# Kernel optimization log

Hardware: AMD Instinct MI355X
Metric: run time of the kernel (lower is better)

## Reference

```python
import jax, jax.numpy as jnp
import numpy as np

HID = 10
IN_DIM = 256
B, H, W = 8, 96, 96


def _conv(x, w, b=None, pad=0):
    y = jax.lax.conv_general_dilated(x, w, (1, 1), [(pad, pad), (pad, pad)],
                                     dimension_numbers=('NCHW', 'OIHW', 'NCHW'))
    return y if b is None else y + b[None, :, None, None]


def _bn(x, g, b):
    # eval-mode InPlaceABN(Sync) with identity running stats -> per-channel affine
    return x * g[None, :, None, None] + b[None, :, None, None]


def _branch(x, w1, g1, b1, w2, g2, b2):
    # Conv3x3 -> BN -> ReLU -> Conv1x1 -> BN -> ReLU  (relation / comp_u / comp_l)
    y = jax.nn.relu(_bn(_conv(x, w1, pad=1), g1, b1))
    return jax.nn.relu(_bn(_conv(y, w2), g2, b2))


def _gru(x, h, gw, gb, cw, cg, cb):
    # ConvGRU with 1x1 kernels
    gates = _conv(jnp.concatenate([x, h], axis=1), gw, gb)
    r = jax.nn.sigmoid(gates[:, 0:1])
    u = jax.nn.sigmoid(gates[:, 1:2])
    cnm = jax.nn.relu(_bn(_conv(jnp.concatenate([x, r * h], axis=1), cw), cg, cb))
    return (1.0 - u) * h + u * cnm


def setup_inputs():
    key = jax.random.key(0)
    ks = iter(jax.random.split(key, 48))

    def nrm(shape, s=0.05):
        return jax.random.normal(next(ks), shape, jnp.float32) * s

    inp = {
        'f_nodes': jax.random.normal(next(ks), (2, B, HID, H, W), jnp.float32),
        'h_nodes': jax.random.normal(next(ks), (3, B, HID, H, W), jnp.float32),
        'p_nodes': jax.random.normal(next(ks), (7, B, HID, H, W), jnp.float32),
        'xh': jax.random.normal(next(ks), (B, IN_DIM, H, W), jnp.float32),
        'f_atts': jax.random.uniform(next(ks), (2, B, 1, H, W), jnp.float32),
        'p_atts': jax.random.uniform(next(ks), (7, B, 1, H, W), jnp.float32),
        # Decomposition.decomp_att: Conv3x3(257->256)+BN+ReLU, Conv1x1(256->2)+bias
        'da_w1': nrm((IN_DIM, IN_DIM + 1, 3, 3)),
        'da_g1': jnp.ones((IN_DIM,), jnp.float32),
        'da_b1': jnp.zeros((IN_DIM,), jnp.float32),
        'da_w2': nrm((2, IN_DIM, 1, 1)),
        'da_b2': jnp.zeros((2,), jnp.float32),
    }
    # relation (shared across children), comp_u, comp_l: Conv3x3(20->10)+BN+ReLU, Conv1x1(10->10)+BN+ReLU
    for p in ('rel', 'cu', 'cl'):
        inp[p + '_w1'] = nrm((HID, 2 * HID, 3, 3))
        inp[p + '_g1'] = jnp.ones((HID,), jnp.float32)
        inp[p + '_b1'] = jnp.zeros((HID,), jnp.float32)
        inp[p + '_w2'] = nrm((HID, HID, 1, 1))
        inp[p + '_g2'] = jnp.ones((HID,), jnp.float32)
        inp[p + '_b2'] = jnp.zeros((HID,), jnp.float32)
    # 3 ConvGRUs (cls_h), 1x1 kernels, stacked on leading dim
    inp['gru_gw'] = nrm((3, 2, 2 * HID, 1, 1))
    inp['gru_gb'] = jnp.zeros((3, 2), jnp.float32)
    inp['gru_cw'] = nrm((3, HID, 2 * HID, 1, 1))
    inp['gru_cg'] = jnp.ones((3, HID), jnp.float32)
    inp['gru_cb'] = jnp.zeros((3, HID), jnp.float32)
    return inp


def reference(f_nodes, h_nodes, p_nodes, xh, f_atts, p_atts,
              da_w1, da_g1, da_b1, da_w2, da_b2,
              rel_w1, rel_g1, rel_b1, rel_w2, rel_g2, rel_b2,
              cu_w1, cu_g1, cu_b1, cu_w2, cu_g2, cu_b2,
              cl_w1, cl_g1, cl_b1, cl_w2, cl_g2, cl_b2,
              gru_gw, gru_gb, gru_cw, gru_cg, gru_cb):
    parent, parent_att = f_nodes[1], f_atts[1]
    # Decomposition of full-body node into 2 half nodes
    dm = _conv(jnp.concatenate([parent_att, xh], axis=1), da_w1, pad=1)
    dm = jax.nn.relu(_bn(dm, da_g1, da_b1))
    dm = _conv(dm, da_w2, da_b2)  # [B, 2, H, W] decomposition map
    datt = jax.nn.softmax(dm, axis=1)
    decomp = [_branch(jnp.concatenate([parent * datt[:, i:i + 1] * parent_att,
                                       h_nodes[1 + i]], axis=1),
                      rel_w1, rel_g1, rel_b1, rel_w2, rel_g2, rel_b2)
              for i in range(2)]
    # node 0: background
    n0 = _gru(f_nodes[0] + p_nodes[0], h_nodes[0],
              gru_gw[0], gru_gb[0], gru_cw[0], gru_cg[0], gru_cb[0])
    # node 1: upper half = composition(upper parts 1-4) + decomposition
    up = jnp.sum(p_nodes[1:5], axis=0) * jnp.sum(p_atts[1:5], axis=0)
    comp_u = _branch(jnp.concatenate([h_nodes[1], up], axis=1),
                     cu_w1, cu_g1, cu_b1, cu_w2, cu_g2, cu_b2)
    n1 = _gru(comp_u + decomp[0], h_nodes[1],
              gru_gw[1], gru_gb[1], gru_cw[1], gru_cg[1], gru_cb[1])
    # node 2: lower half = composition(lower parts 5-6) + decomposition
    lo = jnp.sum(p_nodes[5:7], axis=0) * jnp.sum(p_atts[5:7], axis=0)
    comp_l = _branch(jnp.concatenate([h_nodes[2], lo], axis=1),
                     cl_w1, cl_g1, cl_b1, cl_w2, cl_g2, cl_b2)
    n2 = _gru(comp_l + decomp[1], h_nodes[2],
              gru_gw[2], gru_gb[2], gru_cw[2], gru_cg[2], gru_cb[2])
    return (jnp.stack([n0, n1, n2]), dm)
```

## Files before the change

kernel.cpp:

```cpp
#include <hip/hip_runtime.h>
#include <cstddef>
#include <cstdint>

constexpr int Bn    = 8;
constexpr int Hn    = 96;
constexpr int Wn    = 96;
constexpr int HWn   = Hn * Wn;
constexpr int BHWn  = Bn * HWn;
constexpr int B10HW = Bn * 10 * HWn;

constexpr int XP_COLS        = 100;
constexpr int XP_ROWS        = 100;
constexpr int XP_PLANE       = XP_ROWS * XP_COLS;
constexpr int XP_PLANE_BYTES = XP_PLANE * 16;
constexpr int XP_OCT         = 36;

using short8  = __attribute__((ext_vector_type(8))) short;
using ushort8 = __attribute__((ext_vector_type(8))) unsigned short;
using float4v = __attribute__((ext_vector_type(4))) float;

__device__ __forceinline__ unsigned short f2bf(float f) {
    unsigned u = __builtin_bit_cast(unsigned, f);
    u += 0x7FFFu + ((u >> 16) & 1u);
    return (unsigned short)(u >> 16);
}

__device__ __forceinline__ void async16(const void* g, void* l) {
    auto gp = (__attribute__((address_space(1))) unsigned int*)(uintptr_t)g;
    auto lp = (__attribute__((address_space(3))) unsigned int*)(unsigned)(uintptr_t)l;
    __builtin_amdgcn_global_load_lds(gp, lp, 16, 0, 0);
}

struct BranchW  { const float *w1, *g1, *b1, *w2, *g2, *b2; };
struct BranchW3 { BranchW p[3]; };

struct ConvSmem   { short xs[3][4][194][8]; float part[4][64][2]; };
struct BranchSmem {
    float xt[20][10][34];
    float paSum[340];
    float wlt[9 * 20 * 12];
    float w2l[100], g1l[10], b1l[10], g2l[10], b2l[10];
};
struct GruSmem    { float gwl[40], cwl[200], gbl[2], cgl[10], cbl[10]; };
union FusedSmem { ConvSmem c; BranchSmem b; GruSmem g; };

constexpr int PACKW_BLOCKS = 2592;

__global__ void k_pack(const float* __restrict__ w1, short* __restrict__ wpk,
                       const float* __restrict__ xh, const float* __restrict__ patt,
                       ushort* __restrict__ xp)
{
    if (blockIdx.x < PACKW_BLOCKS) {
        const int o = blockIdx.x * 256 + threadIdx.x;
        const int j    = o & 7;
        const int lane = (o >> 3) & 63;
        const int q    = (o >> 9) & 15;
        const int t    = o >> 13;
        const int co   = q * 16 + (lane & 15);
        const int ci   = (t / 9) * 32 + ((lane >> 4) & 3) * 8 + j;
        const int tap  = t % 9;
        const float f  = (ci < 257) ? w1[((size_t)co * 257 + ci) * 9 + tap] : 0.f;
        wpk[o] = (short)f2bf(f);
    } else {
        const int g  = (blockIdx.x - PACKW_BLOCKS) * 256 + threadIdx.x;
        const int cw = g % XP_COLS;
        int t = g / XP_COLS;
        const int rh = t % XP_ROWS; t /= XP_ROWS;
        const int o  = t % XP_OCT;
        const int b  = t / XP_OCT;
        const int hh = rh - 1, ww = cw - 1;
        const bool inb = ((unsigned)hh < (unsigned)Hn) & ((unsigned)ww < (unsigned)Wn);
        const int off = hh * Wn + ww;
        ushort8 v;
        #pragma unroll
        for (int j = 0; j < 8; ++j) {
            const int ci = o * 8 + j;
            float f = 0.f;
            if (inb && ci < 257)
                f = (ci == 0) ? patt[b * HWn + off]
                              : xh[((size_t)b * 256 + (ci - 1)) * HWn + off];
            v[j] = f2bf(f);
        }
        *(ushort8*)&xp[(size_t)g * 8] = v;
    }
}

__global__ void k_packw(const float* __restrict__ w1, short* __restrict__ wpk)
{
    const int o = blockIdx.x * 256 + threadIdx.x;
    if (o >= 663552) return;
    const int j    = o & 7;
    const int lane = (o >> 3) & 63;
    const int q    = (o >> 9) & 15;
    const int t    = o >> 13;
    const int co   = q * 16 + (lane & 15);
    const int ci   = (t / 9) * 32 + ((lane >> 4) & 3) * 8 + j;
    const int tap  = t % 9;
    const float f  = (ci < 257) ? w1[((size_t)co * 257 + ci) * 9 + tap] : 0.f;
    wpk[o] = (short)f2bf(f);
}

__device__ __forceinline__ void branch_body(
    BranchSmem& S, int z, int bx, int tid, const BranchW3& P,
    const float* __restrict__ parent, const float* __restrict__ h_nodes,
    const float* __restrict__ s01, const float* __restrict__ pn,
    const float* __restrict__ pa, float* __restrict__ bout)
{
    const int pi = (z < 2) ? 0 : (z - 1);
    const BranchW& Pw = P.p[pi];
    for (int idx = tid; idx < 2160; idx += 256) {
        const int co = idx % 12, rem = idx / 12, ci = rem % 20, tap = rem / 20;
        S.wlt[idx] = (co < 10) ? Pw.w1[(co * 20 + ci) * 9 + tap] : 0.f;
    }
    if (tid < 100) S.w2l[tid] = Pw.w2[tid];
    if (tid < 10) {
        S.g1l[tid] = Pw.g1[tid]; S.b1l[tid] = Pw.b1[tid];
        S.g2l[tid] = Pw.g2[tid]; S.b2l[tid] = Pw.b2[tid];
    }

    const int tw = bx % 3, th = (bx / 3) % 12, b = bx / 36;
    const int h0 = th * 8, w0 = tw * 32;

    const float* Ab;
    const float* sc = nullptr;
    const float* Bb = nullptr;
    int k0 = 0, k1 = -1;
    if (z == 0)      { Ab = parent; sc = s01;        Bb = h_nodes + (size_t)1 * B10HW; }
    else if (z == 1) { Ab = parent; sc = s01 + BHWn; Bb = h_nodes + (size_t)2 * B10HW; }
    else if (z == 2) { Ab = h_nodes + (size_t)1 * B10HW; k0 = 1; k1 = 4; }
    else             { Ab = h_nodes + (size_t)2 * B10HW; k0 = 5; k1 = 6; }

    if (z >= 2) {
        for (int idx = tid; idx < 340; idx += 256) {
            const int col = idx % 34, row = idx / 34;
            const int hh = h0 - 1 + row, ww = w0 - 1 + col;
            float s = 0.f;
            if (((unsigned)hh < (unsigned)Hn) & ((unsigned)ww < (unsigned)Wn)) {
                const int off = hh * Wn + ww;
                for (int k = k0; k <= k1; ++k)
                    s += pa[(size_t)(k * Bn + b) * HWn + off];
            }
            S.paSum[idx] = s;
        }
    }
    __syncthreads();

    for (int idx = tid; idx < 6800; idx += 256) {
        const int col = idx % 34, rem = idx / 34, row = rem % 10, ch = rem / 10;
        const int hh = h0 - 1 + row, ww = w0 - 1 + col;
        float v = 0.f;
        if (((unsigned)hh < (unsigned)Hn) & ((unsigned)ww < (unsigned)Wn)) {
            const int off = hh * Wn + ww;
            if (ch < 10) {
                v = Ab[((size_t)b * 10 + ch) * HWn + off];
                if (sc) v *= sc[b * HWn + off];
            } else if (z < 2) {
                v = Bb[((size_t)b * 10 + (ch - 10)) * HWn + off];
            } else {
                float s = 0.f;
                for (int k = k0; k <= k1; ++k)
                    s += pn[((size_t)(k * Bn + b) * 10 + (ch - 10)) * HWn + off];
                v = s * S.paSum[row * 34 + col];
            }
        }
        ((float*)S.xt)[idx] = v;
    }
    __syncthreads();

    const int r = tid >> 5, c = tid & 31;
    float a0 = 0, a1 = 0, a2 = 0, a3 = 0, a4 = 0, a5 = 0, a6 = 0, a7 = 0, a8 = 0, a9 = 0;
    #pragma unroll
    for (int tap = 0; tap < 9; ++tap) {
        const int kh = tap / 3, kw = tap % 3;
        #pragma unroll
        for (int ci = 0; ci < 20; ++ci) {
            const float xv = S.xt[ci][r + kh][c + kw];
            const float4 wA = *(const float4*)&S.wlt[(tap * 20 + ci) * 12];
            const float4 wB = *(const float4*)&S.wlt[(tap * 20 + ci) * 12 + 4];
            const float2 wC = *(const float2*)&S.wlt[(tap * 20 + ci) * 12 + 8];
            a0 = fmaf(wA.x, xv, a0); a1 = fmaf(wA.y, xv, a1);
            a2 = fmaf(wA.z, xv, a2); a3 = fmaf(wA.w, xv, a3);
            a4 = fmaf(wB.x, xv, a4); a5 = fmaf(wB.y, xv, a5);
            a6 = fmaf(wB.z, xv, a6); a7 = fmaf(wB.w, xv, a7);
            a8 = fmaf(wC.x, xv, a8); a9 = fmaf(wC.y, xv, a9);
        }
    }
    float acc[10] = {a0, a1, a2, a3, a4, a5, a6, a7, a8, a9};
    float y[10];
    #pragma unroll
    for (int co = 0; co < 10; ++co)
        y[co] = fmaxf(fmaf(acc[co], S.g1l[co], S.b1l[co]), 0.f);
    const int hw = (h0 + r) * Wn + (w0 + c);
    #pragma unroll
    for (int co = 0; co < 10; ++co) {
        float s = 0.f;
        #pragma unroll
        for (int i = 0; i < 10; ++i) s = fmaf(S.w2l[co * 10 + i], y[i], s);
        s = fmaxf(fmaf(s, S.g2l[co], S.b2l[co]), 0.f);
        bout[(size_t)z * B10HW + ((size_t)b * 10 + co) * HWn + hw] = s;
    }
}

__device__ __forceinline__ void gru_body(
    GruSmem& S, int z, int bx, int tid,
    const float* __restrict__ f_nodes, const float* __restrict__ h_nodes,
    const float* __restrict__ p_nodes, const float* __restrict__ bout,
    const float* __restrict__ gw, const float* __restrict__ gb,
    const float* __restrict__ cw, const float* __restrict__ cg,
    const float* __restrict__ cb, float* __restrict__ out)
{
    if (tid < 40)  S.gwl[tid] = gw[z * 40 + tid];
    if (tid < 200) S.cwl[tid] = cw[z * 200 + tid];
    if (tid < 2)   S.gbl[tid] = gb[z * 2 + tid];
    if (tid < 10) {
        S.cgl[tid] = cg[z * 10 + tid];
        S.cbl[tid] = cb[z * 10 + tid];
    }
    __syncthreads();

    const int p = bx * 256 + tid;
    const int b = p / HWn, hw = p % HWn;
    float x[10], h[10];
    #pragma unroll
    for (int c = 0; c < 10; ++c) {
        const size_t idx = ((size_t)b * 10 + c) * HWn + hw;
        if (z == 0)      x[c] = f_nodes[idx] + p_nodes[idx];
        else if (z == 1) x[c] = bout[(size_t)2 * B10HW + idx] + bout[idx];
        else             x[c] = bout[(size_t)3 * B10HW + idx] + bout[(size_t)1 * B10HW + idx];
        h[c] = h_nodes[(size_t)z * B10HW + idx];
    }
    float g0 = S.gbl[0], g1 = S.gbl[1];
    #pragma unroll
    for (int c = 0; c < 10; ++c) {
        g0 = fmaf(S.gwl[c],      x[c], g0);
        g0 = fmaf(S.gwl[10 + c], h[c], g0);
        g1 = fmaf(S.gwl[20 + c], x[c], g1);
        g1 = fmaf(S.gwl[30 + c], h[c], g1);
    }
    const float r = 1.f / (1.f + expf(-g0));
    const float u = 1.f / (1.f + expf(-g1));
    #pragma unroll
    for (int o = 0; o < 10; ++o) {
        float s = 0.f;
        #pragma unroll
        for (int c = 0; c < 10; ++c) {
            s = fmaf(S.cwl[o * 20 + c],      x[c],     s);
            s = fmaf(S.cwl[o * 20 + 10 + c], r * h[c], s);
        }
        s = fmaxf(fmaf(s, S.cgl[o], S.cbl[o]), 0.f);
        out[(size_t)z * B10HW + ((size_t)b * 10 + o) * HWn + hw] =
            (1.f - u) * h[o] + u * s;
    }
}

constexpr int CONV_BLOCKS = 1152;

__global__ __launch_bounds__(256, 3)
void k_fused(const char* __restrict__ xp, const float* __restrict__ patt,
             const short* __restrict__ wpk, const float* __restrict__ g1,
             const float* __restrict__ b1, const float* __restrict__ w2,
             const float* __restrict__ db2,
             float* __restrict__ dm_out, float* __restrict__ s01,
             BranchW3 P, const float* __restrict__ parent,
             const float* __restrict__ h_nodes, const float* __restrict__ pn,
             const float* __restrict__ pa, float* __restrict__ bout,
             const float* __restrict__ f_nodes, const float* __restrict__ p_nodes,
             const float* __restrict__ gw, const float* __restrict__ gb,
             const float* __restrict__ cw, const float* __restrict__ cg,
             const float* __restrict__ cb, float* __restrict__ out)
{
    __shared__ __align__(16) FusedSmem sm;
    const int tid = threadIdx.x;
    const int bxg = blockIdx.x;

    if (bxg >= CONV_BLOCKS) {
        const int r = bxg - CONV_BLOCKS;
        if (r < 576) {
            const int z = (r < 288) ? 2 : 3;
            branch_body(sm.b, z, (r < 288) ? r : r - 288, tid, P, parent,
                        h_nodes, s01, pn, pa, bout);
        } else {
            gru_body(sm.g, 0, r - 576, tid, f_nodes, h_nodes, p_nodes, bout,
                     gw, gb, cw, cg, cb, out);
        }
        return;
    }

    const int lane = tid & 63;
    const int wid  = tid >> 6;
    const int bx   = bxg;
    const int b    = bx & 7;
    const int r2   = bx >> 3;
    const int wseg = r2 % 3;
    const int hb   = r2 / 3;
    const int h0   = hb * 2, w0 = wseg * 32;
    const int am   = lane & 15;
    const int aq   = lane >> 4;

    int poff[3];
    #pragma unroll
    for (int it = 0; it < 3; ++it) {
        const int pos = it * 64 + lane;
        const int row = pos / 34, col = pos - row * 34;
        poff[it] = ((h0 + row) * XP_COLS + (w0 + col)) * 16;
    }
    const char* xpb = xp + ((size_t)b * XP_OCT + wid) * XP_PLANE_BYTES;

    float4v acc[4][4];
    #pragma unroll
    for (int i = 0; i < 4; ++i)
        #pragma unroll
        for (int j = 0; j < 4; ++j)
            acc[i][j] = float4v{0.f, 0.f, 0.f, 0.f};

    int arow[4], acol[4];
    #pragma unroll
    for (int mt = 0; mt < 4; ++mt) {
        const int m = mt * 16 + am;
        arow[mt] = m >> 5;
        acol[mt] = m & 31;
    }

    auto stageX = [&](int cb, int buf) {
        const char* src = xpb + (size_t)cb * (4 * XP_PLANE_BYTES);
        #pragma unroll
        for (int it = 0; it < 3; ++it)
            async16(src + poff[it], &sm.c.xs[buf][wid][it * 64][0]);
    };

    const short8* wp = (const short8*)wpk;
    const int qb = wid * 4;

    auto loadB = [&](int t, short8 (&dst)[4]) {
        #pragma unroll
        for (int nt = 0; nt < 4; ++nt)
            dst[nt] = wp[((size_t)t * 16 + qb + nt) * 64 + lane];
    };

    stageX(0, 0);
    stageX(1, 1);
    short8 bfr[3][4];
    loadB(0, bfr[0]);
    loadB(1, bfr[1]);

    for (int cb = 0; cb < 9; ++cb) {
        __builtin_amdgcn_sched_barrier(0);
        if (cb < 8) asm volatile("s_waitcnt vmcnt(3)" ::: "memory");
        else        asm volatile("s_waitcnt vmcnt(0)" ::: "memory");
        __builtin_amdgcn_s_barrier();
        __builtin_amdgcn_sched_barrier(0);
        if (cb < 7) stageX(cb + 2, (cb + 2) % 3);

        const int buf = cb % 3;
        #pragma unroll
        for (int tap = 0; tap < 9; ++tap) {
            const int t  = cb * 9 + tap;
            const int tl = (t + 2 <= 80) ? (t + 2) : 80;
            loadB(tl, bfr[(tap + 2) % 3]);
            const int kh = tap / 3, kw = tap % 3;
            short8 afr[4];
            #pragma unroll
            for (int mt = 0; mt < 4; ++mt) {
                const int pos = (arow[mt] + kh) * 34 + (acol[mt] + kw);
                afr[mt] = *(const short8*)&sm.c.xs[buf][aq][pos][0];
            }
            __builtin_amdgcn_s_setprio(1);
            #pragma unroll
            for (int mt = 0; mt < 4; ++mt)
                #pragma unroll
                for (int nt = 0; nt < 4; ++nt)
                    acc[mt][nt] = __builtin_amdgcn_mfma_f32_16x16x32_bf16(
                        afr[mt], bfr[tap % 3][nt], acc[mt][nt], 0, 0, 0);
            __builtin_amdgcn_s_setprio(0);
        }
    }

    float gv[4], bv[4], wa[4], wbv[4];
    #pragma unroll
    for (int nt = 0; nt < 4; ++nt) {
        const int co = wid * 64 + nt * 16 + am;
        gv[nt]  = g1[co];
        bv[nt]  = b1[co];
        wa[nt]  = w2[co];
        wbv[nt] = w2[256 + co];
    }
    #pragma unroll
    for (int mt = 0; mt < 4; ++mt) {
        #pragma unroll
        for (int reg = 0; reg < 4; ++reg) {
            float s0 = 0.f, s1 = 0.f;
            #pragma unroll
            for (int nt = 0; nt < 4; ++nt) {
                const float y = fmaxf(fmaf(acc[mt][nt][reg], gv[nt], bv[nt]), 0.f);
                s0 = fmaf(wa[nt], y, s0);
                s1 = fmaf(wbv[nt], y, s1);
            }
            #pragma unroll
            for (int off = 1; off < 16; off <<= 1) {
                s0 += __shfl_xor(s0, off, 64);
                s1 += __shfl_xor(s1, off, 64);
            }
            if (am == 0) {
                const int m = mt * 16 + aq * 4 + reg;
                sm.c.part[wid][m][0] = s0;
                sm.c.part[wid][m][1] = s1;
            }
        }
    }
    __syncthreads();
    if (tid < 64) {
        const int m = tid, r = m >> 5, c = m & 31;
        const int off = (h0 + r) * Wn + (w0 + c);
        float d0 = sm.c.part[0][m][0] + sm.c.part[1][m][0] + sm.c.part[2][m][0]
                 + sm.c.part[3][m][0] + db2[0];
        float d1 = sm.c.part[0][m][1] + sm.c.part[1][m][1] + sm.c.part[2][m][1]
                 + sm.c.part[3][m][1] + db2[1];
        dm_out[(size_t)(b * 2) * HWn + off]     = d0;
        dm_out[(size_t)(b * 2 + 1) * HWn + off] = d1;
        const float mx = fmaxf(d0, d1);
        const float e0 = expf(d0 - mx), e1 = expf(d1 - mx);
        const float pa2 = patt[b * HWn + off];
        const float inv = pa2 / (e0 + e1);
        s01[b * HWn + off]        = e0 * inv;
        s01[BHWn + b * HWn + off] = e1 * inv;
    }
}

__global__ __launch_bounds__(256)
void k_branch01(BranchW3 P, const float* __restrict__ parent,
                const float* __restrict__ h_nodes, const float* __restrict__ s01,
                const float* __restrict__ pn, const float* __restrict__ pa,
                float* __restrict__ bout)
{
    __shared__ __align__(16) BranchSmem S;
    branch_body(S, blockIdx.y, blockIdx.x, threadIdx.x, P, parent, h_nodes,
                s01, pn, pa, bout);
}

__global__ void k_gru12(const float* __restrict__ f_nodes, const float* __restrict__ h_nodes,
                        const float* __restrict__ p_nodes, const float* __restrict__ bout,
                        const float* __restrict__ gw, const float* __restrict__ gb,
                        const float* __restrict__ cw, const float* __restrict__ cg,
                        const float* __restrict__ cb, float* __restrict__ out)
{
    __shared__ GruSmem S;
    gru_body(S, blockIdx.y + 1, blockIdx.x, threadIdx.x, f_nodes, h_nodes,
             p_nodes, bout, gw, gb, cw, cg, cb, out);
}

__global__ __launch_bounds__(256)
void k_branch_all(BranchW3 P, const float* __restrict__ parent,
                  const float* __restrict__ h_nodes, const float* __restrict__ s01,
                  const float* __restrict__ pn, const float* __restrict__ pa,
                  float* __restrict__ bout)
{
    __shared__ __align__(16) BranchSmem S;
    branch_body(S, blockIdx.y, blockIdx.x, threadIdx.x, P, parent, h_nodes,
                s01, pn, pa, bout);
}

__global__ void k_gru_all(const float* __restrict__ f_nodes, const float* __restrict__ h_nodes,
                          const float* __restrict__ p_nodes, const float* __restrict__ bout,
                          const float* __restrict__ gw, const float* __restrict__ gb,
                          const float* __restrict__ cw, const float* __restrict__ cg,
                          const float* __restrict__ cb, float* __restrict__ out)
{
    __shared__ GruSmem S;
    gru_body(S, blockIdx.y, blockIdx.x, threadIdx.x, f_nodes, h_nodes,
             p_nodes, bout, gw, gb, cw, cg, cb, out);
}

__global__ __launch_bounds__(256, 3)
void k_bigconv3_f(const float* __restrict__ xh, const float* __restrict__ patt,
                  const short* __restrict__ wpk, const float* __restrict__ g1,
                  const float* __restrict__ b1, const float* __restrict__ w2,
                  const float* __restrict__ db2,
                  float* __restrict__ dm_out, float* __restrict__ s01)
{
    __shared__ __align__(16) short xs[2][4][137][8];
    __shared__ float part[4][64][2];

    const int tid  = threadIdx.x;
    const int lane = tid & 63;
    const int wid  = tid >> 6;
    const int bx   = blockIdx.x;
    const int b    = bx & 7;
    const int r2   = bx >> 3;
    const int wseg = r2 % 3;
    const int hb   = r2 / 3;
    const int h0   = hb * 2, w0 = wseg * 32;
    const int am   = lane & 15;
    const int aq   = lane >> 4;

    float4v acc[4][4];
    #pragma unroll
    for (int i = 0; i < 4; ++i)
        #pragma unroll
        for (int j = 0; j < 4; ++j)
            acc[i][j] = float4v{0.f, 0.f, 0.f, 0.f};

    int arow[4], acol[4];
    #pragma unroll
    for (int mt = 0; mt < 4; ++mt) {
        const int m = mt * 16 + am;
        arow[mt] = m >> 5;
        acol[mt] = m & 31;
    }

    auto stageX = [&](int cb, int buf) {
        const int cig0 = cb * 32 + wid * 8;
        for (int pos = lane; pos < 136; pos += 64) {
            const int row = pos / 34, col = pos % 34;
            const int hh = h0 - 1 + row, ww = w0 - 1 + col;
            const bool inb = ((unsigned)hh < (unsigned)Hn) & ((unsigned)ww < (unsigned)Wn);
            const int off = hh * Wn + ww;
            ushort8 v;
            #pragma unroll
            for (int j = 0; j < 8; ++j) {
                const int ci = cig0 + j;
                float f = 0.f;
                if (inb && ci < 257)
                    f = (ci == 0) ? patt[b * HWn + off]
                                  : xh[((size_t)b * 256 + (ci - 1)) * HWn + off];
                v[j] = f2bf(f);
            }
            *(ushort8*)&xs[buf][wid][pos][0] = v;
        }
    };

    const short8* wp = (const short8*)wpk;
    const int qb = wid * 4;

    stageX(0, 0);
    short8 bfr[4], bnx[4];
    #pragma unroll
    for (int nt = 0; nt < 4; ++nt)
        bfr[nt] = wp[(size_t)(qb + nt) * 64 + lane];
    __syncthreads();

    for (int cb = 0; cb < 9; ++cb) {
        const int buf = cb & 1;
        for (int tap = 0; tap < 9; ++tap) {
            const int t = cb * 9 + tap;
            if (t < 80) {
                #pragma unroll
                for (int nt = 0; nt < 4; ++nt)
                    bnx[nt] = wp[((size_t)(t + 1) * 16 + qb + nt) * 64 + lane];
            }
            const int kh = tap / 3, kw = tap % 3;
            short8 afr[4];
            #pragma unroll
            for (int mt = 0; mt < 4; ++mt) {
                const int pos = (arow[mt] + kh) * 34 + (acol[mt] + kw);
                afr[mt] = *(const short8*)&xs[buf][aq][pos][0];
            }
            #pragma unroll
            for (int mt = 0; mt < 4; ++mt)
                #pragma unroll
                for (int nt = 0; nt < 4; ++nt)
                    acc[mt][nt] = __builtin_amdgcn_mfma_f32_16x16x32_bf16(
                        afr[mt], bfr[nt], acc[mt][nt], 0, 0, 0);
            #pragma unroll
            for (int nt = 0; nt < 4; ++nt) bfr[nt] = bnx[nt];
        }
        if (cb < 8) stageX(cb + 1, buf ^ 1);
        __syncthreads();
    }

    float gv[4], bv[4], wa[4], wbv[4];
    #pragma unroll
    for (int nt = 0; nt < 4; ++nt) {
        const int co = wid * 64 + nt * 16 + am;
        gv[nt]  = g1[co];
        bv[nt]  = b1[co];
        wa[nt]  = w2[co];
        wbv[nt] = w2[256 + co];
    }
    #pragma unroll
    for (int mt = 0; mt < 4; ++mt) {
        #pragma unroll
        for (int reg = 0; reg < 4; ++reg) {
            float s0 = 0.f, s1 = 0.f;
            #pragma unroll
            for (int nt = 0; nt < 4; ++nt) {
                const float y = fmaxf(fmaf(acc[mt][nt][reg], gv[nt], bv[nt]), 0.f);
                s0 = fmaf(wa[nt], y, s0);
                s1 = fmaf(wbv[nt], y, s1);
            }
            #pragma unroll
            for (int off = 1; off < 16; off <<= 1) {
                s0 += __shfl_xor(s0, off, 64);
                s1 += __shfl_xor(s1, off, 64);
            }
            if (am == 0) {
                const int m = mt * 16 + aq * 4 + reg;
                part[wid][m][0] = s0;
                part[wid][m][1] = s1;
            }
        }
    }
    __syncthreads();
    if (tid < 64) {
        const int m = tid, r = m >> 5, c = m & 31;
        const int off = (h0 + r) * Wn + (w0 + c);
        float d0 = part[0][m][0] + part[1][m][0] + part[2][m][0] + part[3][m][0] + db2[0];
        float d1 = part[0][m][1] + part[1][m][1] + part[2][m][1] + part[3][m][1] + db2[1];
        dm_out[(size_t)(b * 2) * HWn + off]     = d0;
        dm_out[(size_t)(b * 2 + 1) * HWn + off] = d1;
        const float mx = fmaxf(d0, d1);
        const float e0 = expf(d0 - mx), e1 = expf(d1 - mx);
        const float pa = patt[b * HWn + off];
        const float inv = pa / (e0 + e1);
        s01[b * HWn + off]        = e0 * inv;
        s01[BHWn + b * HWn + off] = e1 * inv;
    }
}

extern "C" void kernel_launch(void* const* d_in, const int* in_sizes, int n_in,
                              void* d_out, int out_size, void* d_ws, size_t ws_size,
                              hipStream_t stream)
{
    (void)in_sizes; (void)n_in; (void)out_size;

    const float* f_nodes = (const float*)d_in[0];
    const float* h_nodes = (const float*)d_in[1];
    const float* p_nodes = (const float*)d_in[2];
    const float* xh      = (const float*)d_in[3];
    const float* f_atts  = (const float*)d_in[4];
    const float* p_atts  = (const float*)d_in[5];
    const float* da_w1   = (const float*)d_in[6];
    const float* da_g1   = (const float*)d_in[7];
    const float* da_b1   = (const float*)d_in[8];
    const float* da_w2   = (const float*)d_in[9];
    const float* da_b2   = (const float*)d_in[10];

    BranchW3 P;
    for (int i = 0; i < 3; ++i) {
        P.p[i].w1 = (const float*)d_in[11 + 6 * i + 0];
        P.p[i].g1 = (const float*)d_in[11 + 6 * i + 1];
        P.p[i].b1 = (const float*)d_in[11 + 6 * i + 2];
        P.p[i].w2 = (const float*)d_in[11 + 6 * i + 3];
        P.p[i].g2 = (const float*)d_in[11 + 6 * i + 4];
        P.p[i].b2 = (const float*)d_in[11 + 6 * i + 5];
    }
    const float* gru_gw = (const float*)d_in[29];
    const float* gru_gb = (const float*)d_in[30];
    const float* gru_cw = (const float*)d_in[31];
    const float* gru_cg = (const float*)d_in[32];
    const float* gru_cb = (const float*)d_in[33];

    float* out    = (float*)d_out;
    float* dm_out = out + (size_t)3 * B10HW;

    float* ws   = (float*)d_ws;
    float* s01  = ws;
    float* bout = s01 + 2 * BHWn;
    short* wpk  = (short*)bout;
    const size_t XP_OFF_B = ((size_t)(2 * BHWn) + 4 * (size_t)B10HW) * 4;
    char*  xp   = (char*)d_ws + XP_OFF_B;
    const size_t WS_NEED = XP_OFF_B + (size_t)Bn * XP_OCT * XP_PLANE_BYTES;
    const bool use_packed = ws_size >= WS_NEED;

    const float* patt   = f_atts + BHWn;
    const float* parent = f_nodes + B10HW;

    if (use_packed) {
        k_pack<<<dim3(PACKW_BLOCKS + 11250), 256, 0, stream>>>(da_w1, wpk, xh, patt,
                                                               (ushort*)xp);
        k_fused<<<dim3(CONV_BLOCKS + 576 + 288), 256, 0, stream>>>(
            xp, patt, wpk, da_g1, da_b1, da_w2, da_b2, dm_out, s01,
            P, parent, h_nodes, p_nodes, p_atts, bout,
            f_nodes, p_nodes, gru_gw, gru_gb, gru_cw, gru_cg, gru_cb, out);
        k_branch01<<<dim3(288, 2), 256, 0, stream>>>(P, parent, h_nodes, s01,
                                                     p_nodes, p_atts, bout);
        k_gru12<<<dim3(288, 2), 256, 0, stream>>>(f_nodes, h_nodes, p_nodes, bout,
                                                  gru_gw, gru_gb, gru_cw, gru_cg,
                                                  gru_cb, out);
    } else {
        k_packw<<<dim3(2592), 256, 0, stream>>>(da_w1, wpk);
        k_bigconv3_f<<<dim3(1152), 256, 0, stream>>>(xh, patt, wpk, da_g1, da_b1,
                                                     da_w2, da_b2, dm_out, s01);
        k_branch_all<<<dim3(288, 4), 256, 0, stream>>>(P, parent, h_nodes, s01,
                                                       p_nodes, p_atts, bout);
        k_gru_all<<<dim3(288, 3), 256, 0, stream>>>(f_nodes, h_nodes, p_nodes, bout,
                                                    gru_gw, gru_gb, gru_cw, gru_cg,
                                                    gru_cb, out);
    }
}
```

Baseline: 360.2 us.

## Split attention channel out of bf16 MFMA conv into separate fp32 rank-1 term

The 257-channel 3x3 conv had been padded to 288 input channels (9 chunks of 32), and the extra attention channel alone forced a ninth MFMA chunk. The attention channel now gets its own packed fp32 weights and is staged into LDS per block, then added to the accumulators as a 9-tap scalar FMA after the MFMA loop. The main loop therefore runs 8 chunks over exactly 256 channels, and the packed input shrinks from 36 to 32 octets, cutting pack traffic and MFMA work by about a ninth. The cost is extra scalar FMAs and LDS reads in the epilogue, plus more register pressure from the 36 per-thread weights.

After: 367.8 us. +2.1%, slower.

```diff
diff --git a/kernel.cpp b/kernel.cpp
--- a/kernel.cpp
+++ b/kernel.cpp
@@ -13,7 +13,7 @@
 constexpr int XP_ROWS        = 100;
 constexpr int XP_PLANE       = XP_ROWS * XP_COLS;
 constexpr int XP_PLANE_BYTES = XP_PLANE * 16;
-constexpr int XP_OCT         = 36;
+constexpr int XP_OCT         = 32;
 
 using short8  = __attribute__((ext_vector_type(8))) short;
 using ushort8 = __attribute__((ext_vector_type(8))) unsigned short;
@@ -34,7 +34,11 @@
 struct BranchW  { const float *w1, *g1, *b1, *w2, *g2, *b2; };
 struct BranchW3 { BranchW p[3]; };
 
-struct ConvSmem   { short xs[3][4][194][8]; float part[4][64][2]; };
+struct ConvSmem {
+    short xs[3][4][194][8];
+    float part[4][64][2];
+    float pt[4][34];
+};
 struct BranchSmem {
     float xt[20][10][34];
     float paSum[340];
@@ -44,11 +48,13 @@
 struct GruSmem    { float gwl[40], cwl[200], gbl[2], cgl[10], cbl[10]; };
 union FusedSmem { ConvSmem c; BranchSmem b; GruSmem g; };
 
-constexpr int PACKW_BLOCKS = 2592;
+constexpr int PACKW_BLOCKS  = 2304;
+constexpr int PACKPAT_BLOCKS = 9;
+constexpr int PACKX_BLOCKS  = 10000;
 
 __global__ void k_pack(const float* __restrict__ w1, short* __restrict__ wpk,
-                       const float* __restrict__ xh, const float* __restrict__ patt,
-                       ushort* __restrict__ xp)
+                       float* __restrict__ wpat,
+                       const float* __restrict__ xh, ushort* __restrict__ xp)
 {
     if (blockIdx.x < PACKW_BLOCKS) {
         const int o = blockIdx.x * 256 + threadIdx.x;
@@ -57,12 +63,18 @@
         const int q    = (o >> 9) & 15;
         const int t    = o >> 13;
         const int co   = q * 16 + (lane & 15);
-        const int ci   = (t / 9) * 32 + ((lane >> 4) & 3) * 8 + j;
+        const int ci   = (t / 9) * 32 + ((lane >> 4) & 3) * 8 + j + 1;
         const int tap  = t % 9;
-        const float f  = (ci < 257) ? w1[((size_t)co * 257 + ci) * 9 + tap] : 0.f;
-        wpk[o] = (short)f2bf(f);
+        wpk[o] = (short)f2bf(w1[((size_t)co * 257 + ci) * 9 + tap]);
+    } else if (blockIdx.x < PACKW_BLOCKS + PACKPAT_BLOCKS) {
+        const int idx = (blockIdx.x - PACKW_BLOCKS) * 256 + threadIdx.x;
+        if (idx < 2304) {
+            const int co = idx / 9, tap = idx % 9;
+            wpat[idx] = w1[(size_t)co * 257 * 9 + tap];
+        }
     } else {
-        const int g  = (blockIdx.x - PACKW_BLOCKS) * 256 + threadIdx.x;
+        const int g  = (blockIdx.x - PACKW_BLOCKS - PACKPAT_BLOCKS) * 256
+                     + threadIdx.x;
         const int cw = g % XP_COLS;
         int t = g / XP_COLS;
         const int rh = t % XP_ROWS; t /= XP_ROWS;
@@ -75,10 +87,7 @@
         #pragma unroll
         for (int j = 0; j < 8; ++j) {
             const int ci = o * 8 + j;
-            float f = 0.f;
-            if (inb && ci < 257)
-                f = (ci == 0) ? patt[b * HWn + off]
-                              : xh[((size_t)b * 256 + (ci - 1)) * HWn + off];
+            float f = inb ? xh[((size_t)b * 256 + ci) * HWn + off] : 0.f;
             v[j] = f2bf(f);
         }
         *(ushort8*)&xp[(size_t)g * 8] = v;
@@ -257,7 +266,8 @@
 
 __global__ __launch_bounds__(256, 3)
 void k_fused(const char* __restrict__ xp, const float* __restrict__ patt,
-             const short* __restrict__ wpk, const float* __restrict__ g1,
+             const short* __restrict__ wpk, const float* __restrict__ wpat,
+             const float* __restrict__ g1,
              const float* __restrict__ b1, const float* __restrict__ w2,
              const float* __restrict__ db2,
              float* __restrict__ dm_out, float* __restrict__ s01,
@@ -286,9 +296,9 @@
         return;
     }
 
+    const int bx   = bxg;
     const int lane = tid & 63;
     const int wid  = tid >> 6;
-    const int bx   = bxg;
     const int b    = bx & 7;
     const int r2   = bx >> 3;
     const int wseg = r2 % 3;
@@ -297,6 +307,16 @@
     const int am   = lane & 15;
     const int aq   = lane >> 4;
 
+    for (int idx = tid; idx < 136; idx += 256) {
+        const int row = idx / 34, col = idx % 34;
+        const int hh = h0 - 1 + row, ww = w0 - 1 + col;
+        float v = 0.f;
+        if (((unsigned)hh < (unsigned)Hn) & ((unsigned)ww < (unsigned)Wn))
+            v = patt[b * HWn + hh * Wn + ww];
+        sm.c.pt[row][col] = v;
+    }
+    asm volatile("s_waitcnt lgkmcnt(0)" ::: "memory");
+
     int poff[3];
     #pragma unroll
     for (int it = 0; it < 3; ++it) {
@@ -343,19 +363,19 @@
     loadB(0, bfr[0]);
     loadB(1, bfr[1]);
 
-    for (int cb = 0; cb < 9; ++cb) {
+    for (int cb = 0; cb < 8; ++cb) {
         __builtin_amdgcn_sched_barrier(0);
-        if (cb < 8) asm volatile("s_waitcnt vmcnt(3)" ::: "memory");
+        if (cb < 7) asm volatile("s_waitcnt vmcnt(3)" ::: "memory");
         else        asm volatile("s_waitcnt vmcnt(0)" ::: "memory");
         __builtin_amdgcn_s_barrier();
         __builtin_amdgcn_sched_barrier(0);
-        if (cb < 7) stageX(cb + 2, (cb + 2) % 3);
+        if (cb < 6) stageX(cb + 2, (cb + 2) % 3);
 
         const int buf = cb % 3;
         #pragma unroll
         for (int tap = 0; tap < 9; ++tap) {
             const int t  = cb * 9 + tap;
-            const int tl = (t + 2 <= 80) ? (t + 2) : 80;
+            const int tl = (t + 2 <= 71) ? (t + 2) : 71;
             loadB(tl, bfr[(tap + 2) % 3]);
             const int kh = tap / 3, kw = tap % 3;
             short8 afr[4];
@@ -372,6 +392,35 @@
                     acc[mt][nt] = __builtin_amdgcn_mfma_f32_16x16x32_bf16(
                         afr[mt], bfr[tap % 3][nt], acc[mt][nt], 0, 0, 0);
             __builtin_amdgcn_s_setprio(0);
+        }
+    }
+
+    float wpr[4][9];
+    #pragma unroll
+    for (int nt = 0; nt < 4; ++nt) {
+        const int co = wid * 64 + nt * 16 + am;
+        #pragma unroll
+        for (int tap = 0; tap < 9; ++tap)
+            wpr[nt][tap] = wpat[co * 9 + tap];
+    }
+    #pragma unroll
+    for (int mt = 0; mt < 4; ++mt) {
+        #pragma unroll
+        for (int reg = 0; reg < 4; ++reg) {
+            const int m = mt * 16 + aq * 4 + reg;
+            const int r = m >> 5, cc = m & 31;
+            float pv[9];
+            #pragma unroll
+            for (int tap = 0; tap < 9; ++tap)
+                pv[tap] = sm.c.pt[r + tap / 3][cc + tap % 3];
+            #pragma unroll
+            for (int nt = 0; nt < 4; ++nt) {
+                float s = 0.f;
+                #pragma unroll
+                for (int tap = 0; tap < 9; ++tap)
+                    s = fmaf(wpr[nt][tap], pv[tap], s);
+                acc[mt][nt][reg] += s;
+            }
         }
     }
 
@@ -656,6 +705,7 @@
     float* s01  = ws;
     float* bout = s01 + 2 * BHWn;
     short* wpk  = (short*)bout;
+    float* wpat = (float*)(wpk + 589824);
     const size_t XP_OFF_B = ((size_t)(2 * BHWn) + 4 * (size_t)B10HW) * 4;
     char*  xp   = (char*)d_ws + XP_OFF_B;
     const size_t WS_NEED = XP_OFF_B + (size_t)Bn * XP_OCT * XP_PLANE_BYTES;
@@ -665,10 +715,10 @@
     const float* parent = f_nodes + B10HW;
 
     if (use_packed) {
-        k_pack<<<dim3(PACKW_BLOCKS + 11250), 256, 0, stream>>>(da_w1, wpk, xh, patt,
-                                                               (ushort*)xp);
+        k_pack<<<dim3(PACKW_BLOCKS + PACKPAT_BLOCKS + PACKX_BLOCKS), 256, 0, stream>>>(
+            da_w1, wpk, wpat, xh, (ushort*)xp);
         k_fused<<<dim3(CONV_BLOCKS + 576 + 288), 256, 0, stream>>>(
-            xp, patt, wpk, da_g1, da_b1, da_w2, da_b2, dm_out, s01,
+            xp, patt, wpk, wpat, da_g1, da_b1, da_w2, da_b2, dm_out, s01,
             P, parent, h_nodes, p_nodes, p_atts, bout,
             f_nodes, p_nodes, gru_gw, gru_gb, gru_cw, gru_cg, gru_cb, out);
         k_branch01<<<dim3(288, 2), 256, 0, stream>>>(P, parent, h_nodes, s01,
```
